# Optimization experiments

Hardware: AMD Instinct MI355X
Metric: run time of the kernel (lower is better)

The kernel has to match this reference:

```python
import jax, jax.numpy as jnp
import numpy as np

N_NODES = 50000
BN_EPS = 1e-5


def setup_inputs() -> dict:
    key = jax.random.key(0)
    ks = jax.random.split(key, 16)
    N, IN, H, OUT, E = N_NODES, 512, 128, 64, 800000
    s = lambda fi, fo: 1.0 / np.sqrt(fi)
    inp = {
        'x': jax.random.normal(ks[0], (N, IN), dtype=jnp.float32),
        'edge_index': jax.random.randint(ks[1], (2, E), 0, N, dtype=jnp.int32),
        # mlpA: Linear(N -> H)
        'WA': jax.random.uniform(ks[2], (H, N), jnp.float32, -s(N, H), s(N, H)),
        'bA': jax.random.uniform(ks[3], (H,), jnp.float32, -s(N, H), s(N, H)),
        # mlpX: Linear(IN -> H)
        'WX': jax.random.uniform(ks[4], (H, IN), jnp.float32, -s(IN, H), s(IN, H)),
        'bX': jax.random.uniform(ks[5], (H,), jnp.float32, -s(IN, H), s(IN, H)),
        # W: Linear(2H -> H)
        'W': jax.random.uniform(ks[6], (H, 2 * H), jnp.float32, -s(2 * H, H), s(2 * H, H)),
        'bW': jax.random.uniform(ks[7], (H,), jnp.float32, -s(2 * H, H), s(2 * H, H)),
        # mlp_final layer 1: Linear(H -> H) + BN
        'Wf1': jax.random.uniform(ks[8], (H, H), jnp.float32, -s(H, H), s(H, H)),
        'bf1': jax.random.uniform(ks[9], (H,), jnp.float32, -s(H, H), s(H, H)),
        'gamma': jnp.ones((H,), jnp.float32),
        'beta': jnp.zeros((H,), jnp.float32),
        # mlp_final layer 2: Linear(H -> OUT)
        'Wf2': jax.random.uniform(ks[10], (OUT, H), jnp.float32, -s(H, OUT), s(H, OUT)),
        'bf2': jax.random.uniform(ks[11], (OUT,), jnp.float32, -s(H, OUT), s(H, OUT)),
    }
    return inp


def _batchnorm(x, gamma, beta):
    # training-mode BN over the node/batch axis (biased variance, as in torch)
    mean = jnp.mean(x, axis=0)
    var = jnp.var(x, axis=0)
    return (x - mean) * jax.lax.rsqrt(var + BN_EPS) * gamma + beta


def reference(x, edge_index, WA, bA, WX, bX, W, bW, Wf1, bf1, gamma, beta, Wf2, bf2):
    row, col = edge_index[0], edge_index[1]
    row = row - row.min()
    # xA = A @ WA.T + bA  where A[i,j]=1 per (row,col) edge (duplicates sum).
    # Equivalent SpMM: gather columns of WA at `col`, segment-sum into `row`.
    xA = jax.ops.segment_sum(WA.T[col], row, num_segments=N_NODES) + bA  # [N, H]
    xX = x @ WX.T + bX  # [N, H]
    h = jnp.concatenate([xA, xX], axis=-1) @ W.T + bW  # [N, H]
    h = jax.nn.relu(h + xA + xX)
    # mlp_final (num_layers=2): Linear -> ReLU -> BN -> (dropout off) -> Linear
    h = jax.nn.relu(h @ Wf1.T + bf1)
    h = _batchnorm(h, gamma, beta)
    out = h @ Wf2.T + bf2  # [N, OUT]
    return out
```

## Files before the change

### kernel.cpp

```cpp
#include <hip/hip_runtime.h>

typedef __bf16 bf16_t;
typedef __bf16 bf16x8 __attribute__((ext_vector_type(8)));
typedef float f32x4 __attribute__((ext_vector_type(4)));

#define IN_DIM 512
#define H_DIM 128
#define OUT_DIM 64
#define BN_EPS 1e-5f
#define SCAN_BLK 2048

#define MFMA(a, b, c) __builtin_amdgcn_mfma_f32_16x16x32_bf16(a, b, c, 0, 0, 0)

__device__ __forceinline__ float ld_adapt(const void* p, size_t i, int isbf) {
    return isbf ? (float)((const bf16_t*)p)[i] : ((const float*)p)[i];
}

__device__ __forceinline__ void split8(const float* p, bf16x8& hi, bf16x8& lo) {
    f32x4 v0 = *(const f32x4*)p;
    f32x4 v1 = *(const f32x4*)(p + 4);
#pragma unroll
    for (int i = 0; i < 8; ++i) {
        float f = (i < 4) ? v0[i] : v1[i - 4];
        bf16_t h = (bf16_t)f;
        hi[i] = h;
        lo[i] = (bf16_t)(f - (float)h);
    }
}

__device__ __forceinline__ unsigned short bf16_bits(float f) {
    bf16_t h = (bf16_t)f;
    return __builtin_bit_cast(unsigned short, h);
}

__device__ __forceinline__ float2 bf2_unpack(unsigned v) {
    bf16_t lo = __builtin_bit_cast(bf16_t, (unsigned short)(v & 0xffffu));
    bf16_t hi = __builtin_bit_cast(bf16_t, (unsigned short)(v >> 16));
    return float2{(float)lo, (float)hi};
}

__global__ void k_init(const void* bA, const void* bX, const void* bW, const void* bf1,
                       const void* gamma, const void* beta, const void* bf2,
                       float* __restrict__ dst, int* __restrict__ flag) {
    __shared__ int s_isbf;
    if (threadIdx.x == 0) {
        unsigned u = *(const unsigned*)gamma;
        int f = (u == 0x3F803F80u) ? 1 : 0;
        *flag = f;
        s_isbf = f;
    }
    __syncthreads();
    int isbf = s_isbf;
    int t = threadIdx.x;
    dst[t] = ld_adapt(bA, t, isbf);
    dst[128 + t] = ld_adapt(bX, t, isbf);
    dst[256 + t] = ld_adapt(bW, t, isbf);
    dst[384 + t] = ld_adapt(bf1, t, isbf);
    dst[512 + t] = ld_adapt(gamma, t, isbf);
    dst[640 + t] = ld_adapt(beta, t, isbf);
    if (t < OUT_DIM) dst[768 + t] = ld_adapt(bf2, t, isbf);
}

__global__ __launch_bounds__(256) void k_transpose(const void* __restrict__ WA,
                                                   float* __restrict__ WAT, int N,
                                                   const int* __restrict__ flag) {
    __shared__ float t[64][130];
    int isbf = *flag;
    int n0 = blockIdx.x * 64;
    int tid = threadIdx.x;
#pragma unroll
    for (int i = 0; i < 32; ++i) {
        int lin = i * 256 + tid;
        int h = lin >> 6, nl = lin & 63;
        int n = n0 + nl;
        t[nl][h] = (n < N) ? ld_adapt(WA, (size_t)h * N + n, isbf) : 0.f;
    }
    __syncthreads();
    if (isbf) {
#pragma unroll
        for (int i = 0; i < 16; ++i) {
            int lin = i * 256 + tid;
            int nl = lin >> 6, hp = lin & 63;
            int n = n0 + nl;
            if (n < N) {
                unsigned u0 = bf16_bits(t[nl][hp * 2]);
                unsigned u1 = bf16_bits(t[nl][hp * 2 + 1]);
                ((unsigned*)WAT)[(size_t)n * 64 + hp] = u0 | (u1 << 16);
            }
        }
    } else {
#pragma unroll
        for (int i = 0; i < 32; ++i) {
            int lin = i * 256 + tid;
            int nl = lin >> 7, h = lin & 127;
            int n = n0 + nl;
            if (n < N) WAT[(size_t)n * H_DIM + h] = t[nl][h];
        }
    }
}

__global__ __launch_bounds__(256) void k_prep(const int* __restrict__ rows, int E,
                                              int* __restrict__ bmin, int* __restrict__ cnt,
                                              int* __restrict__ rank) {
    __shared__ int sm[4];
    int i = blockIdx.x * 256 + threadIdx.x;
    int m = 0x7fffffff;
    if (i < E) {
        int r = rows[i];
        m = r;
        rank[i] = atomicAdd(&cnt[r], 1);
    }
    for (int off = 32; off; off >>= 1) m = min(m, __shfl_xor(m, off, 64));
    if ((threadIdx.x & 63) == 0) sm[threadIdx.x >> 6] = m;
    __syncthreads();
    if (threadIdx.x == 0)
        bmin[blockIdx.x] = min(min(sm[0], sm[1]), min(sm[2], sm[3]));
}

__global__ __launch_bounds__(256) void k_scan1(const int* __restrict__ cnt,
                                               int* __restrict__ offs,
                                               int* __restrict__ bsum, int N) {
    __shared__ int ts[256];
    int base = blockIdx.x * SCAN_BLK;
    int t = threadIdx.x;
    int v[8], s = 0;
#pragma unroll
    for (int i = 0; i < 8; ++i) {
        int idx = base + t * 8 + i;
        v[i] = (idx < N) ? cnt[idx] : 0;
        s += v[i];
    }
    ts[t] = s;
    __syncthreads();
    for (int off = 1; off < 256; off <<= 1) {
        int x = (t >= off) ? ts[t - off] : 0;
        __syncthreads();
        ts[t] += x;
        __syncthreads();
    }
    int run = ts[t] - s;
#pragma unroll
    for (int i = 0; i < 8; ++i) {
        int idx = base + t * 8 + i;
        if (idx < N) offs[idx] = run;
        run += v[i];
    }
    if (t == 255) bsum[blockIdx.x] = ts[255];
}

__global__ __launch_bounds__(256) void k_scan2(int* __restrict__ bsum, int* __restrict__ offs,
                                               int NB, int N, const int* __restrict__ bmin,
                                               int nbmin, int* __restrict__ minbuf) {
    __shared__ int sm[256];
    int t = threadIdx.x;
    int m = 0x7fffffff;
    for (int i = t; i < nbmin; i += 256) m = min(m, bmin[i]);
    sm[t] = m;
    __syncthreads();
    for (int off = 128; off; off >>= 1) {
        if (t < off) sm[t] = min(sm[t], sm[t + off]);
        __syncthreads();
    }
    if (t == 0) {
        *minbuf = sm[0];
        int run = 0;
        for (int b = 0; b < NB; ++b) {
            int v = bsum[b];
            bsum[b] = run;
            run += v;
        }
        offs[N] = run;
    }
}

__global__ __launch_bounds__(256) void k_scan3(int* __restrict__ offs, const int* __restrict__ bsum,
                                               int N) {
    int i = blockIdx.x * 256 + threadIdx.x;
    if (i >= N) return;
    offs[i] += bsum[i / SCAN_BLK];
}

__global__ __launch_bounds__(256) void k_build(const int* __restrict__ rows,
                                               const int* __restrict__ cols, int E,
                                               const int* __restrict__ offs,
                                               const int* __restrict__ rank,
                                               int* __restrict__ scol) {
    int i = blockIdx.x * 256 + threadIdx.x;
    if (i >= E) return;
    int r = rows[i];
    int pos = offs[r] + rank[i];
    scol[pos] = cols[i];
}

__global__ __launch_bounds__(256) void k_gather(const int* __restrict__ offs,
                                                const int* __restrict__ scol,
                                                const float* __restrict__ WAT,
                                                const float* __restrict__ bA_f,
                                                const int* __restrict__ minbuf,
                                                const int* __restrict__ flag,
                                                float* __restrict__ xA, int N) {
    int wave = threadIdx.x >> 6, lane = threadIdx.x & 63;
    int r = blockIdx.x * 4 + wave;
    if (r >= N) return;
    int b = r + *minbuf;
    int isbf = *flag;
    int s = 0, e = 0;
    if (b < N) {
        s = offs[b];
        e = offs[b + 1];
    }
    float2 a0 = {0.f, 0.f}, a1 = {0.f, 0.f};
    int i = s;
    if (isbf) {
        const unsigned* Wb = (const unsigned*)WAT;
        for (; i + 3 < e; i += 4) {
            int c0 = scol[i], c1 = scol[i + 1], c2 = scol[i + 2], c3 = scol[i + 3];
            unsigned v0 = Wb[(size_t)c0 * 64 + lane];
            unsigned v1 = Wb[(size_t)c1 * 64 + lane];
            unsigned v2 = Wb[(size_t)c2 * 64 + lane];
            unsigned v3 = Wb[(size_t)c3 * 64 + lane];
            float2 w0 = bf2_unpack(v0), w1 = bf2_unpack(v1);
            float2 w2 = bf2_unpack(v2), w3 = bf2_unpack(v3);
            a0.x += w0.x + w2.x; a0.y += w0.y + w2.y;
            a1.x += w1.x + w3.x; a1.y += w1.y + w3.y;
        }
        for (; i < e; ++i) {
            float2 w = bf2_unpack(Wb[(size_t)scol[i] * 64 + lane]);
            a0.x += w.x; a0.y += w.y;
        }
    } else {
        for (; i + 3 < e; i += 4) {
            int c0 = scol[i], c1 = scol[i + 1], c2 = scol[i + 2], c3 = scol[i + 3];
            float2 w0 = *(const float2*)(WAT + (size_t)c0 * H_DIM + lane * 2);
            float2 w1 = *(const float2*)(WAT + (size_t)c1 * H_DIM + lane * 2);
            float2 w2 = *(const float2*)(WAT + (size_t)c2 * H_DIM + lane * 2);
            float2 w3 = *(const float2*)(WAT + (size_t)c3 * H_DIM + lane * 2);
            a0.x += w0.x + w2.x; a0.y += w0.y + w2.y;
            a1.x += w1.x + w3.x; a1.y += w1.y + w3.y;
        }
        for (; i < e; ++i) {
            int c = scol[i];
            float2 w = *(const float2*)(WAT + (size_t)c * H_DIM + lane * 2);
            a0.x += w.x; a0.y += w.y;
        }
    }
    float2 bias = *(const float2*)(bA_f + lane * 2);
    float2 out = {a0.x + a1.x + bias.x, a0.y + a1.y + bias.y};
    *(float2*)(xA + (size_t)r * H_DIM + lane * 2) = out;
}

__device__ __forceinline__ void pack_frag(const void* __restrict__ W, bf16_t* __restrict__ hi,
                                          bf16_t* __restrict__ lo, int K, int NC,
                                          int addres, int isbf, int f, int lane) {
    int ks = f / (NC >> 4), nt = f % (NC >> 4);
    int n = nt * 16 + (lane & 15);
    int k0 = ks * 32 + (lane >> 4) * 8;
    bf16_t* dh = hi + (size_t)f * 512 + lane * 8;
    bf16_t* dl = lo + (size_t)f * 512 + lane * 8;
#pragma unroll
    for (int j = 0; j < 8; ++j) {
        int kk = k0 + j;
        float v = ld_adapt(W, (size_t)n * K + kk, isbf);
        if (addres && (kk == n || kk == n + H_DIM)) v += 1.f;
        bf16_t h = (bf16_t)v;
        dh[j] = h;
        dl[j] = (bf16_t)(v - (float)h);
    }
}

__global__ __launch_bounds__(256) void k_pack3(const void* WX, bf16_t* WXh, bf16_t* WXl,
                                               const void* W, bf16_t* Wh, bf16_t* Wl,
                                               const void* Wf1, bf16_t* Wf1h, bf16_t* Wf1l,
                                               const int* __restrict__ flag) {
    int g = blockIdx.x * 256 + threadIdx.x;
    int f = g >> 6, lane = g & 63;
    int isbf = *flag;
    if (f < 128)
        pack_frag(WX, WXh, WXl, IN_DIM, H_DIM, 0, isbf, f, lane);
    else if (f < 192)
        pack_frag(W, Wh, Wl, 2 * H_DIM, H_DIM, isbf ? 0 : 1, isbf, f - 128, lane);
    else if (f < 224)
        pack_frag(Wf1, Wf1h, Wf1l, H_DIM, H_DIM, 0, isbf, f - 192, lane);
}

template <int ISBF>
__device__ __forceinline__ void fuseA_body(
    const void* __restrict__ x, const float* __restrict__ xAf,
    const bf16_t* __restrict__ WXh, const bf16_t* __restrict__ WXl,
    const bf16_t* __restrict__ Wh, const bf16_t* __restrict__ Wl,
    const bf16_t* __restrict__ Wf1h, const bf16_t* __restrict__ Wf1l,
    const float* __restrict__ smallf, float* __restrict__ h2, int M,
    float* __restrict__ ax, float* __restrict__ ls_sum, float* __restrict__ ls_sq) {
    int tid = threadIdx.x;
    int wave = tid >> 6, lane = tid & 63, l16 = lane & 15, quad = lane >> 4;
    int mbase = blockIdx.x * 64 + wave * 16;
    int r0 = min(mbase + l16, M - 1);
    const float* bX = smallf + 128;
    const float* bW = smallf + 256;
    const float* bf1 = smallf + 384;

    f32x4 acc[8];
#pragma unroll
    for (int nt = 0; nt < 8; ++nt) acc[nt] = f32x4{0.f, 0.f, 0.f, 0.f};
    if (ISBF) {
        size_t offx = (size_t)r0 * IN_DIM + quad * 8;
        for (int ks = 0; ks < 16; ++ks) {
            bf16x8 ah = *(const bf16x8*)((const bf16_t*)x + offx + ks * 32);
            const bf16_t* bhp = WXh + (size_t)ks * 8 * 512 + lane * 8;
#pragma unroll
            for (int nt = 0; nt < 8; ++nt) {
                bf16x8 bh = *(const bf16x8*)(bhp + nt * 512);
                acc[nt] = MFMA(ah, bh, acc[nt]);
            }
        }
    } else {
        size_t offx = (size_t)r0 * IN_DIM + quad * 8;
        for (int ks = 0; ks < 16; ++ks) {
            bf16x8 ah, al;
            split8((const float*)x + offx + ks * 32, ah, al);
            const bf16_t* bhp = WXh + (size_t)ks * 8 * 512 + lane * 8;
            const bf16_t* blp = WXl + (size_t)ks * 8 * 512 + lane * 8;
#pragma unroll
            for (int nt = 0; nt < 8; ++nt) {
                bf16x8 bh = *(const bf16x8*)(bhp + nt * 512);
                bf16x8 bl = *(const bf16x8*)(blp + nt * 512);
                acc[nt] = MFMA(ah, bh, acc[nt]);
                acc[nt] = MFMA(ah, bl, acc[nt]);
                acc[nt] = MFMA(al, bh, acc[nt]);
            }
        }
    }
#pragma unroll
    for (int nt = 0; nt < 8; ++nt) {
        int col = nt * 16 + l16;
        float b = bX[col];
#pragma unroll
        for (int r = 0; r < 4; ++r) {
            int lr = quad * 4 + r;
            ax[lr * 132 + col] = acc[nt][r] + b;
        }
    }

#pragma unroll
    for (int nt = 0; nt < 8; ++nt) acc[nt] = f32x4{0.f, 0.f, 0.f, 0.f};
    for (int ks = 0; ks < 8; ++ks) {
        bf16x8 ah, al;
        if (ks < 4)
            split8(xAf + (size_t)r0 * H_DIM + ks * 32 + quad * 8, ah, al);
        else
            split8(ax + l16 * 132 + (ks - 4) * 32 + quad * 8, ah, al);
        const bf16_t* bhp = Wh + (size_t)ks * 8 * 512 + lane * 8;
        if (ISBF) {
#pragma unroll
            for (int nt = 0; nt < 8; ++nt) {
                bf16x8 bh = *(const bf16x8*)(bhp + nt * 512);
                acc[nt] = MFMA(ah, bh, acc[nt]);
                acc[nt] = MFMA(al, bh, acc[nt]);
            }
        } else {
            const bf16_t* blp = Wl + (size_t)ks * 8 * 512 + lane * 8;
#pragma unroll
            for (int nt = 0; nt < 8; ++nt) {
                bf16x8 bh = *(const bf16x8*)(bhp + nt * 512);
                bf16x8 bl = *(const bf16x8*)(blp + nt * 512);
                acc[nt] = MFMA(ah, bh, acc[nt]);
                acc[nt] = MFMA(ah, bl, acc[nt]);
                acc[nt] = MFMA(al, bh, acc[nt]);
            }
        }
    }
    if (ISBF) {
#pragma unroll
        for (int nt = 0; nt < 8; ++nt) {
            int col = nt * 16 + l16;
            float b = bW[col];
#pragma unroll
            for (int r = 0; r < 4; ++r) {
                int lr = quad * 4 + r;
                int rr = min(mbase + lr, M - 1);
                float resid = xAf[(size_t)rr * H_DIM + col] + ax[lr * 132 + col];
                ax[lr * 132 + col] = fmaxf(acc[nt][r] + b + resid, 0.f);
            }
        }
    } else {
#pragma unroll
        for (int nt = 0; nt < 8; ++nt) {
            int col = nt * 16 + l16;
            float b = bW[col];
#pragma unroll
            for (int r = 0; r < 4; ++r) {
                int lr = quad * 4 + r;
                ax[lr * 132 + col] = fmaxf(acc[nt][r] + b, 0.f);
            }
        }
    }

#pragma unroll
    for (int nt = 0; nt < 8; ++nt) acc[nt] = f32x4{0.f, 0.f, 0.f, 0.f};
    for (int ks = 0; ks < 4; ++ks) {
        bf16x8 ah, al;
        split8(ax + l16 * 132 + ks * 32 + quad * 8, ah, al);
        const bf16_t* bhp = Wf1h + (size_t)ks * 8 * 512 + lane * 8;
        if (ISBF) {
#pragma unroll
            for (int nt = 0; nt < 8; ++nt) {
                bf16x8 bh = *(const bf16x8*)(bhp + nt * 512);
                acc[nt] = MFMA(ah, bh, acc[nt]);
                acc[nt] = MFMA(al, bh, acc[nt]);
            }
        } else {
            const bf16_t* blp = Wf1l + (size_t)ks * 8 * 512 + lane * 8;
#pragma unroll
            for (int nt = 0; nt < 8; ++nt) {
                bf16x8 bh = *(const bf16x8*)(bhp + nt * 512);
                bf16x8 bl = *(const bf16x8*)(blp + nt * 512);
                acc[nt] = MFMA(ah, bh, acc[nt]);
                acc[nt] = MFMA(ah, bl, acc[nt]);
                acc[nt] = MFMA(al, bh, acc[nt]);
            }
        }
    }
#pragma unroll
    for (int nt = 0; nt < 8; ++nt) {
        int col = nt * 16 + l16;
        float b = bf1[col];
        float s = 0.f, s2 = 0.f;
#pragma unroll
        for (int r = 0; r < 4; ++r) {
            int row = mbase + quad * 4 + r;
            if (row < M) {
                float v = fmaxf(acc[nt][r] + b, 0.f);
                h2[(size_t)row * H_DIM + col] = v;
                s += v;
                s2 += v * v;
            }
        }
        s += __shfl_xor(s, 16, 64);
        s += __shfl_xor(s, 32, 64);
        s2 += __shfl_xor(s2, 16, 64);
        s2 += __shfl_xor(s2, 32, 64);
        if (quad == 0) {
            atomicAdd(&ls_sum[col], s);
            atomicAdd(&ls_sq[col], s2);
        }
    }
}

__global__ __launch_bounds__(256) void k_fuseA(
    const void* __restrict__ x, const float* __restrict__ xAf,
    const bf16_t* __restrict__ WXh, const bf16_t* __restrict__ WXl,
    const bf16_t* __restrict__ Wh, const bf16_t* __restrict__ Wl,
    const bf16_t* __restrict__ Wf1h, const bf16_t* __restrict__ Wf1l,
    const float* __restrict__ smallf, float* __restrict__ h2,
    double* __restrict__ sums, double* __restrict__ sumsq,
    const int* __restrict__ flag, int M) {
    __shared__ float axx[4][16 * 132];
    __shared__ float ls_sum[H_DIM], ls_sq[H_DIM];
    int tid = threadIdx.x;
    if (tid < H_DIM) {
        ls_sum[tid] = 0.f;
        ls_sq[tid] = 0.f;
    }
    __syncthreads();
    float* ax = axx[tid >> 6];
    if (*flag)
        fuseA_body<1>(x, xAf, WXh, WXl, Wh, Wl, Wf1h, Wf1l, smallf, h2, M, ax, ls_sum, ls_sq);
    else
        fuseA_body<0>(x, xAf, WXh, WXl, Wh, Wl, Wf1h, Wf1l, smallf, h2, M, ax, ls_sum, ls_sq);
    __syncthreads();
    if (tid < H_DIM) {
        atomicAdd(&sums[tid], (double)ls_sum[tid]);
        atomicAdd(&sumsq[tid], (double)ls_sq[tid]);
    }
}

__global__ __launch_bounds__(256) void k_packB(
    const void* __restrict__ Wf2, const float* __restrict__ smallf,
    const double* __restrict__ sums, const double* __restrict__ sumsq,
    bf16_t* __restrict__ W2h, bf16_t* __restrict__ W2l,
    float* __restrict__ b2g, const int* __restrict__ flag, int M) {
    __shared__ float aw[H_DIM], cw[H_DIM];
    int t = threadIdx.x;
    int isbf = *flag;
    const float* gamma_f = smallf + 512;
    const float* beta_f = smallf + 640;
    const float* bf2_f = smallf + 768;
    if (t < H_DIM) {
        double mean = sums[t] / (double)M;
        double var = sumsq[t] / (double)M - mean * mean;
        if (var < 0) var = 0;
        float a = gamma_f[t] * rsqrtf((float)var + BN_EPS);
        aw[t] = a;
        cw[t] = beta_f[t] - (float)mean * a;
    }
    __syncthreads();
    if (t < OUT_DIM) {
        float acc = bf2_f[t];
        for (int j = 0; j < H_DIM; ++j) acc += ld_adapt(Wf2, (size_t)t * H_DIM + j, isbf) * cw[j];
        b2g[t] = acc;
    }
    for (int u = t; u < 1024; u += 256) {
        int f = u >> 6, ln = u & 63;
        int ks = f >> 2, nt = f & 3;
        int n = nt * 16 + (ln & 15);
        int k0 = ks * 32 + (ln >> 4) * 8;
#pragma unroll
        for (int j = 0; j < 8; ++j) {
            float v = ld_adapt(Wf2, (size_t)n * H_DIM + k0 + j, isbf) * aw[k0 + j];
            bf16_t h = (bf16_t)v;
            W2h[f * 512 + ln * 8 + j] = h;
            W2l[f * 512 + ln * 8 + j] = (bf16_t)(v - (float)h);
        }
    }
}

__global__ __launch_bounds__(256) void k_fuseB(
    const float* __restrict__ h2, const bf16_t* __restrict__ W2h,
    const bf16_t* __restrict__ W2l, const float* __restrict__ b2g,
    void* __restrict__ outv, const int* __restrict__ flag, int M) {
    int t = threadIdx.x;
    int isbf = *flag;
    int wave = t >> 6, lane = t & 63, l16 = lane & 15, quad = lane >> 4;
    int mbase = blockIdx.x * 64 + wave * 16;
    int r0 = min(mbase + l16, M - 1);
    f32x4 acc4[4];
#pragma unroll
    for (int nt = 0; nt < 4; ++nt) acc4[nt] = f32x4{0.f, 0.f, 0.f, 0.f};
    for (int ks = 0; ks < 4; ++ks) {
        bf16x8 ah, al;
        split8(h2 + (size_t)r0 * H_DIM + ks * 32 + quad * 8, ah, al);
#pragma unroll
        for (int nt = 0; nt < 4; ++nt) {
            bf16x8 bh = *(const bf16x8*)(W2h + (ks * 4 + nt) * 512 + lane * 8);
            bf16x8 bl = *(const bf16x8*)(W2l + (ks * 4 + nt) * 512 + lane * 8);
            acc4[nt] = MFMA(ah, bh, acc4[nt]);
            acc4[nt] = MFMA(ah, bl, acc4[nt]);
            acc4[nt] = MFMA(al, bh, acc4[nt]);
        }
    }
#pragma unroll
    for (int nt = 0; nt < 4; ++nt) {
        int col = nt * 16 + l16;
        float b = b2g[col];
#pragma unroll
        for (int r = 0; r < 4; ++r) {
            int row = mbase + quad * 4 + r;
            if (row < M) {
                float v = acc4[nt][r] + b;
                if (isbf)
                    ((bf16_t*)outv)[(size_t)row * OUT_DIM + col] = (bf16_t)v;
                else
                    ((float*)outv)[(size_t)row * OUT_DIM + col] = v;
            }
        }
    }
}

extern "C" void kernel_launch(void* const* d_in, const int* in_sizes, int n_in,
                              void* d_out, int out_size, void* d_ws, size_t ws_size,
                              hipStream_t stream) {
    const void* x = d_in[0];
    const int* ei = (const int*)d_in[1];
    const void* WA = d_in[2];
    const void* bA = d_in[3];
    const void* WX = d_in[4];
    const void* bX = d_in[5];
    const void* W = d_in[6];
    const void* bW = d_in[7];
    const void* Wf1 = d_in[8];
    const void* bf1 = d_in[9];
    const void* gamma = d_in[10];
    const void* beta = d_in[11];
    const void* Wf2 = d_in[12];
    const void* bf2 = d_in[13];

    const int N = in_sizes[0] / IN_DIM;
    const int E = in_sizes[1] / 2;
    const int* rows = ei;
    const int* cols = ei + E;
    const int eblocks = (E + 255) / 256;

    char* ws = (char*)d_ws;
    size_t off = 0;
    auto alloc = [&](size_t bytes) {
        char* p = ws + off;
        off += (bytes + 255) & ~(size_t)255;
        return p;
    };
    int* flag = (int*)alloc(4);
    int* minbuf = (int*)alloc(4);
    float* smallf = (float*)alloc(832 * 4);
    double* sums = (double*)alloc(2 * H_DIM * 8);
    double* sumsq = sums + H_DIM;
    bf16_t* WXp_h = (bf16_t*)alloc((size_t)IN_DIM * H_DIM * 2);
    bf16_t* WXp_l = (bf16_t*)alloc((size_t)IN_DIM * H_DIM * 2);
    bf16_t* Wp_h = (bf16_t*)alloc((size_t)256 * H_DIM * 2);
    bf16_t* Wp_l = (bf16_t*)alloc((size_t)256 * H_DIM * 2);
    bf16_t* Wf1p_h = (bf16_t*)alloc((size_t)H_DIM * H_DIM * 2);
    bf16_t* Wf1p_l = (bf16_t*)alloc((size_t)H_DIM * H_DIM * 2);
    bf16_t* W2h = (bf16_t*)alloc((size_t)16 * 512 * 2);
    bf16_t* W2l = (bf16_t*)alloc((size_t)16 * 512 * 2);
    float* b2g = (float*)alloc(OUT_DIM * 4);
    int* cnt = (int*)alloc((size_t)N * 4);
    int* offs = (int*)alloc(((size_t)N + 1) * 4);
    int* rank = (int*)alloc((size_t)E * 4);
    int* bsum = (int*)alloc(64 * 4);
    int* bmin = (int*)alloc((size_t)eblocks * 4);
    int* scol = (int*)alloc((size_t)E * 4);
    float* WAT = (float*)alloc((size_t)N * H_DIM * 4);
    float* xAf = (float*)alloc((size_t)N * H_DIM * 4);
    float* h2 = WAT;

    float* bA_f = smallf + 0;

    hipMemsetAsync(cnt, 0, (size_t)N * 4, stream);
    hipMemsetAsync(sums, 0, 2 * H_DIM * 8, stream);

    k_init<<<1, 128, 0, stream>>>(bA, bX, bW, bf1, gamma, beta, bf2, smallf, flag);
    k_transpose<<<(N + 63) / 64, 256, 0, stream>>>(WA, WAT, N, flag);
    k_pack3<<<56, 256, 0, stream>>>(WX, WXp_h, WXp_l, W, Wp_h, Wp_l, Wf1, Wf1p_h, Wf1p_l, flag);

    k_prep<<<eblocks, 256, 0, stream>>>(rows, E, bmin, cnt, rank);
    int NB = (N + SCAN_BLK - 1) / SCAN_BLK;
    k_scan1<<<NB, 256, 0, stream>>>(cnt, offs, bsum, N);
    k_scan2<<<1, 256, 0, stream>>>(bsum, offs, NB, N, bmin, eblocks, minbuf);
    k_scan3<<<(N + 255) / 256, 256, 0, stream>>>(offs, bsum, N);
    k_build<<<eblocks, 256, 0, stream>>>(rows, cols, E, offs, rank, scol);
    k_gather<<<(N + 3) / 4, 256, 0, stream>>>(offs, scol, WAT, bA_f, minbuf, flag, xAf, N);

    int fblocks = (N + 63) / 64;
    k_fuseA<<<fblocks, 256, 0, stream>>>(x, xAf, WXp_h, WXp_l, Wp_h, Wp_l, Wf1p_h, Wf1p_l,
                                         smallf, h2, sums, sumsq, flag, N);
    k_packB<<<1, 256, 0, stream>>>(Wf2, smallf, sums, sumsq, W2h, W2l, b2g, flag, N);
    k_fuseB<<<fblocks, 256, 0, stream>>>(h2, W2h, W2l, b2g, d_out, flag, N);
}
```

Measured before the change: 457.2 us.

## Split fused MLP block across waves by output columns with banked BN atomics

Each k_fuseA block now handles 16 rows instead of 64, and its four waves split the 128 output columns (two 16-column tiles each) instead of each wave owning its own 16 rows. The shared activation tile is shared across the block with __syncthreads between stages, and launch bounds request higher occupancy. Per-block shared-memory BN reduction is replaced by direct double atomics into 8 banks indexed by block, and k_packB sums the banks. This lowers registers per thread and raises block count and occupancy, but every wave now reloads the same x rows, and the change adds barriers and four times as many global atomics.

Result: slower. 472.1 us (+3.3%).

```diff
diff --git a/kernel.cpp b/kernel.cpp
--- a/kernel.cpp
+++ b/kernel.cpp
@@ -289,147 +289,128 @@
     const bf16_t* __restrict__ WXh, const bf16_t* __restrict__ WXl,
     const bf16_t* __restrict__ Wh, const bf16_t* __restrict__ Wl,
     const bf16_t* __restrict__ Wf1h, const bf16_t* __restrict__ Wf1l,
-    const float* __restrict__ smallf, float* __restrict__ h2, int M,
-    float* __restrict__ ax, float* __restrict__ ls_sum, float* __restrict__ ls_sq) {
+    const float* __restrict__ smallf, float* __restrict__ h2,
+    double* __restrict__ sums, double* __restrict__ sumsq, int M,
+    float* __restrict__ ax) {
     int tid = threadIdx.x;
     int wave = tid >> 6, lane = tid & 63, l16 = lane & 15, quad = lane >> 4;
-    int mbase = blockIdx.x * 64 + wave * 16;
+    int mbase = blockIdx.x * 16;
     int r0 = min(mbase + l16, M - 1);
+    int nt0 = wave * 2;
     const float* bX = smallf + 128;
     const float* bW = smallf + 256;
     const float* bf1 = smallf + 384;
 
-    f32x4 acc[8];
-#pragma unroll
-    for (int nt = 0; nt < 8; ++nt) acc[nt] = f32x4{0.f, 0.f, 0.f, 0.f};
-    if (ISBF) {
-        size_t offx = (size_t)r0 * IN_DIM + quad * 8;
-        for (int ks = 0; ks < 16; ++ks) {
-            bf16x8 ah = *(const bf16x8*)((const bf16_t*)x + offx + ks * 32);
-            const bf16_t* bhp = WXh + (size_t)ks * 8 * 512 + lane * 8;
-#pragma unroll
-            for (int nt = 0; nt < 8; ++nt) {
-                bf16x8 bh = *(const bf16x8*)(bhp + nt * 512);
-                acc[nt] = MFMA(ah, bh, acc[nt]);
-            }
-        }
-    } else {
+    f32x4 acc[2];
+    acc[0] = f32x4{0.f, 0.f, 0.f, 0.f};
+    acc[1] = f32x4{0.f, 0.f, 0.f, 0.f};
+
+    {
         size_t offx = (size_t)r0 * IN_DIM + quad * 8;
         for (int ks = 0; ks < 16; ++ks) {
             bf16x8 ah, al;
-            split8((const float*)x + offx + ks * 32, ah, al);
-            const bf16_t* bhp = WXh + (size_t)ks * 8 * 512 + lane * 8;
-            const bf16_t* blp = WXl + (size_t)ks * 8 * 512 + lane * 8;
-#pragma unroll
-            for (int nt = 0; nt < 8; ++nt) {
-                bf16x8 bh = *(const bf16x8*)(bhp + nt * 512);
-                bf16x8 bl = *(const bf16x8*)(blp + nt * 512);
-                acc[nt] = MFMA(ah, bh, acc[nt]);
-                acc[nt] = MFMA(ah, bl, acc[nt]);
-                acc[nt] = MFMA(al, bh, acc[nt]);
-            }
-        }
-    }
-#pragma unroll
-    for (int nt = 0; nt < 8; ++nt) {
-        int col = nt * 16 + l16;
+            if (ISBF) {
+                ah = *(const bf16x8*)((const bf16_t*)x + offx + ks * 32);
+            } else {
+                split8((const float*)x + offx + ks * 32, ah, al);
+            }
+#pragma unroll
+            for (int ntl = 0; ntl < 2; ++ntl) {
+                size_t fo = (size_t)(ks * 8 + nt0 + ntl) * 512 + lane * 8;
+                bf16x8 bh = *(const bf16x8*)(WXh + fo);
+                acc[ntl] = MFMA(ah, bh, acc[ntl]);
+                if (!ISBF) {
+                    bf16x8 bl = *(const bf16x8*)(WXl + fo);
+                    acc[ntl] = MFMA(ah, bl, acc[ntl]);
+                    acc[ntl] = MFMA(al, bh, acc[ntl]);
+                }
+            }
+        }
+    }
+#pragma unroll
+    for (int ntl = 0; ntl < 2; ++ntl) {
+        int col = (nt0 + ntl) * 16 + l16;
         float b = bX[col];
 #pragma unroll
         for (int r = 0; r < 4; ++r) {
             int lr = quad * 4 + r;
-            ax[lr * 132 + col] = acc[nt][r] + b;
-        }
-    }
-
-#pragma unroll
-    for (int nt = 0; nt < 8; ++nt) acc[nt] = f32x4{0.f, 0.f, 0.f, 0.f};
+            ax[lr * 132 + col] = acc[ntl][r] + b;
+        }
+    }
+    __syncthreads();
+
+    acc[0] = f32x4{0.f, 0.f, 0.f, 0.f};
+    acc[1] = f32x4{0.f, 0.f, 0.f, 0.f};
     for (int ks = 0; ks < 8; ++ks) {
         bf16x8 ah, al;
         if (ks < 4)
             split8(xAf + (size_t)r0 * H_DIM + ks * 32 + quad * 8, ah, al);
         else
             split8(ax + l16 * 132 + (ks - 4) * 32 + quad * 8, ah, al);
-        const bf16_t* bhp = Wh + (size_t)ks * 8 * 512 + lane * 8;
-        if (ISBF) {
-#pragma unroll
-            for (int nt = 0; nt < 8; ++nt) {
-                bf16x8 bh = *(const bf16x8*)(bhp + nt * 512);
-                acc[nt] = MFMA(ah, bh, acc[nt]);
-                acc[nt] = MFMA(al, bh, acc[nt]);
-            }
-        } else {
-            const bf16_t* blp = Wl + (size_t)ks * 8 * 512 + lane * 8;
-#pragma unroll
-            for (int nt = 0; nt < 8; ++nt) {
-                bf16x8 bh = *(const bf16x8*)(bhp + nt * 512);
-                bf16x8 bl = *(const bf16x8*)(blp + nt * 512);
-                acc[nt] = MFMA(ah, bh, acc[nt]);
-                acc[nt] = MFMA(ah, bl, acc[nt]);
-                acc[nt] = MFMA(al, bh, acc[nt]);
-            }
-        }
-    }
-    if (ISBF) {
-#pragma unroll
-        for (int nt = 0; nt < 8; ++nt) {
-            int col = nt * 16 + l16;
-            float b = bW[col];
-#pragma unroll
-            for (int r = 0; r < 4; ++r) {
-                int lr = quad * 4 + r;
+#pragma unroll
+        for (int ntl = 0; ntl < 2; ++ntl) {
+            size_t fo = (size_t)(ks * 8 + nt0 + ntl) * 512 + lane * 8;
+            bf16x8 bh = *(const bf16x8*)(Wh + fo);
+            if (ISBF) {
+                acc[ntl] = MFMA(ah, bh, acc[ntl]);
+                acc[ntl] = MFMA(al, bh, acc[ntl]);
+            } else {
+                bf16x8 bl = *(const bf16x8*)(Wl + fo);
+                acc[ntl] = MFMA(ah, bh, acc[ntl]);
+                acc[ntl] = MFMA(ah, bl, acc[ntl]);
+                acc[ntl] = MFMA(al, bh, acc[ntl]);
+            }
+        }
+    }
+    __syncthreads();
+#pragma unroll
+    for (int ntl = 0; ntl < 2; ++ntl) {
+        int col = (nt0 + ntl) * 16 + l16;
+        float b = bW[col];
+#pragma unroll
+        for (int r = 0; r < 4; ++r) {
+            int lr = quad * 4 + r;
+            float v = acc[ntl][r] + b;
+            if (ISBF) {
                 int rr = min(mbase + lr, M - 1);
-                float resid = xAf[(size_t)rr * H_DIM + col] + ax[lr * 132 + col];
-                ax[lr * 132 + col] = fmaxf(acc[nt][r] + b + resid, 0.f);
-            }
-        }
-    } else {
-#pragma unroll
-        for (int nt = 0; nt < 8; ++nt) {
-            int col = nt * 16 + l16;
-            float b = bW[col];
-#pragma unroll
-            for (int r = 0; r < 4; ++r) {
-                int lr = quad * 4 + r;
-                ax[lr * 132 + col] = fmaxf(acc[nt][r] + b, 0.f);
-            }
-        }
-    }
-
-#pragma unroll
-    for (int nt = 0; nt < 8; ++nt) acc[nt] = f32x4{0.f, 0.f, 0.f, 0.f};
+                v += xAf[(size_t)rr * H_DIM + col] + ax[lr * 132 + col];
+            }
+            ax[lr * 132 + col] = fmaxf(v, 0.f);
+        }
+    }
+    __syncthreads();
+
+    acc[0] = f32x4{0.f, 0.f, 0.f, 0.f};
+    acc[1] = f32x4{0.f, 0.f, 0.f, 0.f};
     for (int ks = 0; ks < 4; ++ks) {
         bf16x8 ah, al;
         split8(ax + l16 * 132 + ks * 32 + quad * 8, ah, al);
-        const bf16_t* bhp = Wf1h + (size_t)ks * 8 * 512 + lane * 8;
-        if (ISBF) {
-#pragma unroll
-            for (int nt = 0; nt < 8; ++nt) {
-                bf16x8 bh = *(const bf16x8*)(bhp + nt * 512);
-                acc[nt] = MFMA(ah, bh, acc[nt]);
-                acc[nt] = MFMA(al, bh, acc[nt]);
-            }
-        } else {
-            const bf16_t* blp = Wf1l + (size_t)ks * 8 * 512 + lane * 8;
-#pragma unroll
-            for (int nt = 0; nt < 8; ++nt) {
-                bf16x8 bh = *(const bf16x8*)(bhp + nt * 512);
-                bf16x8 bl = *(const bf16x8*)(blp + nt * 512);
-                acc[nt] = MFMA(ah, bh, acc[nt]);
-                acc[nt] = MFMA(ah, bl, acc[nt]);
-                acc[nt] = MFMA(al, bh, acc[nt]);
-            }
-        }
-    }
-#pragma unroll
-    for (int nt = 0; nt < 8; ++nt) {
-        int col = nt * 16 + l16;
+#pragma unroll
+        for (int ntl = 0; ntl < 2; ++ntl) {
+            size_t fo = (size_t)(ks * 8 + nt0 + ntl) * 512 + lane * 8;
+            bf16x8 bh = *(const bf16x8*)(Wf1h + fo);
+            if (ISBF) {
+                acc[ntl] = MFMA(ah, bh, acc[ntl]);
+                acc[ntl] = MFMA(al, bh, acc[ntl]);
+            } else {
+                bf16x8 bl = *(const bf16x8*)(Wf1l + fo);
+                acc[ntl] = MFMA(ah, bh, acc[ntl]);
+                acc[ntl] = MFMA(ah, bl, acc[ntl]);
+                acc[ntl] = MFMA(al, bh, acc[ntl]);
+            }
+        }
+    }
+    int bank = (blockIdx.x & 7) * H_DIM;
+#pragma unroll
+    for (int ntl = 0; ntl < 2; ++ntl) {
+        int col = (nt0 + ntl) * 16 + l16;
         float b = bf1[col];
         float s = 0.f, s2 = 0.f;
 #pragma unroll
         for (int r = 0; r < 4; ++r) {
             int row = mbase + quad * 4 + r;
             if (row < M) {
-                float v = fmaxf(acc[nt][r] + b, 0.f);
+                float v = fmaxf(acc[ntl][r] + b, 0.f);
                 h2[(size_t)row * H_DIM + col] = v;
                 s += v;
                 s2 += v * v;
@@ -440,13 +421,13 @@
         s2 += __shfl_xor(s2, 16, 64);
         s2 += __shfl_xor(s2, 32, 64);
         if (quad == 0) {
-            atomicAdd(&ls_sum[col], s);
-            atomicAdd(&ls_sq[col], s2);
-        }
-    }
-}
-
-__global__ __launch_bounds__(256) void k_fuseA(
+            atomicAdd(&sums[bank + col], (double)s);
+            atomicAdd(&sumsq[bank + col], (double)s2);
+        }
+    }
+}
+
+__global__ __launch_bounds__(256, 8) void k_fuseA(
     const void* __restrict__ x, const float* __restrict__ xAf,
     const bf16_t* __restrict__ WXh, const bf16_t* __restrict__ WXl,
     const bf16_t* __restrict__ Wh, const bf16_t* __restrict__ Wl,
@@ -454,24 +435,11 @@
     const float* __restrict__ smallf, float* __restrict__ h2,
     double* __restrict__ sums, double* __restrict__ sumsq,
     const int* __restrict__ flag, int M) {
-    __shared__ float axx[4][16 * 132];
-    __shared__ float ls_sum[H_DIM], ls_sq[H_DIM];
-    int tid = threadIdx.x;
-    if (tid < H_DIM) {
-        ls_sum[tid] = 0.f;
-        ls_sq[tid] = 0.f;
-    }
-    __syncthreads();
-    float* ax = axx[tid >> 6];
+    __shared__ float ax[16 * 132];
     if (*flag)
-        fuseA_body<1>(x, xAf, WXh, WXl, Wh, Wl, Wf1h, Wf1l, smallf, h2, M, ax, ls_sum, ls_sq);
+        fuseA_body<1>(x, xAf, WXh, WXl, Wh, Wl, Wf1h, Wf1l, smallf, h2, sums, sumsq, M, ax);
     else
-        fuseA_body<0>(x, xAf, WXh, WXl, Wh, Wl, Wf1h, Wf1l, smallf, h2, M, ax, ls_sum, ls_sq);
-    __syncthreads();
-    if (tid < H_DIM) {
-        atomicAdd(&sums[tid], (double)ls_sum[tid]);
-        atomicAdd(&sumsq[tid], (double)ls_sq[tid]);
-    }
+        fuseA_body<0>(x, xAf, WXh, WXl, Wh, Wl, Wf1h, Wf1l, smallf, h2, sums, sumsq, M, ax);
 }
 
 __global__ __launch_bounds__(256) void k_packB(
@@ -486,8 +454,14 @@
     const float* beta_f = smallf + 640;
     const float* bf2_f = smallf + 768;
     if (t < H_DIM) {
-        double mean = sums[t] / (double)M;
-        double var = sumsq[t] / (double)M - mean * mean;
+        double ssum = 0.0, ssq = 0.0;
+#pragma unroll
+        for (int bk = 0; bk < 8; ++bk) {
+            ssum += sums[bk * H_DIM + t];
+            ssq += sumsq[bk * H_DIM + t];
+        }
+        double mean = ssum / (double)M;
+        double var = ssq / (double)M - mean * mean;
         if (var < 0) var = 0;
         float a = gamma_f[t] * rsqrtf((float)var + BN_EPS);
         aw[t] = a;
@@ -590,8 +564,8 @@
     int* flag = (int*)alloc(4);
     int* minbuf = (int*)alloc(4);
     float* smallf = (float*)alloc(832 * 4);
-    double* sums = (double*)alloc(2 * H_DIM * 8);
-    double* sumsq = sums + H_DIM;
+    double* sums = (double*)alloc(2 * 8 * H_DIM * 8);
+    double* sumsq = sums + 8 * H_DIM;
     bf16_t* WXp_h = (bf16_t*)alloc((size_t)IN_DIM * H_DIM * 2);
     bf16_t* WXp_l = (bf16_t*)alloc((size_t)IN_DIM * H_DIM * 2);
     bf16_t* Wp_h = (bf16_t*)alloc((size_t)256 * H_DIM * 2);
@@ -614,7 +588,7 @@
     float* bA_f = smallf + 0;
 
     hipMemsetAsync(cnt, 0, (size_t)N * 4, stream);
-    hipMemsetAsync(sums, 0, 2 * H_DIM * 8, stream);
+    hipMemsetAsync(sums, 0, 2 * 8 * H_DIM * 8, stream);
 
     k_init<<<1, 128, 0, stream>>>(bA, bX, bW, bf1, gamma, beta, bf2, smallf, flag);
     k_transpose<<<(N + 63) / 64, 256, 0, stream>>>(WA, WAT, N, flag);
@@ -628,9 +602,10 @@
     k_build<<<eblocks, 256, 0, stream>>>(rows, cols, E, offs, rank, scol);
     k_gather<<<(N + 3) / 4, 256, 0, stream>>>(offs, scol, WAT, bA_f, minbuf, flag, xAf, N);
 
-    int fblocks = (N + 63) / 64;
-    k_fuseA<<<fblocks, 256, 0, stream>>>(x, xAf, WXp_h, WXp_l, Wp_h, Wp_l, Wf1p_h, Wf1p_l,
-                                         smallf, h2, sums, sumsq, flag, N);
+    int fblocksA = (N + 15) / 16;
+    k_fuseA<<<fblocksA, 256, 0, stream>>>(x, xAf, WXp_h, WXp_l, Wp_h, Wp_l, Wf1p_h, Wf1p_l,
+                                          smallf, h2, sums, sumsq, flag, N);
     k_packB<<<1, 256, 0, stream>>>(Wf2, smallf, sums, sumsq, W2h, W2l, b2g, flag, N);
-    k_fuseB<<<fblocks, 256, 0, stream>>>(h2, W2h, W2l, b2g, d_out, flag, N);
-}
+    int fblocksB = (N + 63) / 64;
+    k_fuseB<<<fblocksB, 256, 0, stream>>>(h2, W2h, W2l, b2g, d_out, flag, N);
+}
```

## Process two 16-row tiles per wave in fused MLP kernel to reuse weight fragments

Applied to the files above, without the earlier changes.

Each wave in k_fuseA now computes 32 rows instead of 16, holding two sets of accumulators so every loaded weight fragment (hi/lo) feeds two MFMAs. Blocks shrink to 128 threads (2 waves) while still covering 64 rows, halving total weight fragment loads from global/L2. The cost is doubled accumulator register pressure (64 extra VGPRs), which may reduce occupancy, and fewer waves per block.

Result: faster. 435.1 us (-4.8%).

```diff
diff --git a/kernel.cpp b/kernel.cpp
--- a/kernel.cpp
+++ b/kernel.cpp
@@ -293,40 +293,46 @@
     float* __restrict__ ax, float* __restrict__ ls_sum, float* __restrict__ ls_sq) {
     int tid = threadIdx.x;
     int wave = tid >> 6, lane = tid & 63, l16 = lane & 15, quad = lane >> 4;
-    int mbase = blockIdx.x * 64 + wave * 16;
+    int mbase = blockIdx.x * 64 + wave * 32;
     int r0 = min(mbase + l16, M - 1);
+    int r1 = min(mbase + 16 + l16, M - 1);
     const float* bX = smallf + 128;
     const float* bW = smallf + 256;
     const float* bf1 = smallf + 384;
 
-    f32x4 acc[8];
-#pragma unroll
-    for (int nt = 0; nt < 8; ++nt) acc[nt] = f32x4{0.f, 0.f, 0.f, 0.f};
-    if (ISBF) {
-        size_t offx = (size_t)r0 * IN_DIM + quad * 8;
+    f32x4 acc0[8], acc1[8];
+#pragma unroll
+    for (int nt = 0; nt < 8; ++nt) {
+        acc0[nt] = f32x4{0.f, 0.f, 0.f, 0.f};
+        acc1[nt] = f32x4{0.f, 0.f, 0.f, 0.f};
+    }
+
+    {
+        size_t offx0 = (size_t)r0 * IN_DIM + quad * 8;
+        size_t offx1 = (size_t)r1 * IN_DIM + quad * 8;
         for (int ks = 0; ks < 16; ++ks) {
-            bf16x8 ah = *(const bf16x8*)((const bf16_t*)x + offx + ks * 32);
+            bf16x8 ah0, al0, ah1, al1;
+            if (ISBF) {
+                ah0 = *(const bf16x8*)((const bf16_t*)x + offx0 + ks * 32);
+                ah1 = *(const bf16x8*)((const bf16_t*)x + offx1 + ks * 32);
+            } else {
+                split8((const float*)x + offx0 + ks * 32, ah0, al0);
+                split8((const float*)x + offx1 + ks * 32, ah1, al1);
+            }
             const bf16_t* bhp = WXh + (size_t)ks * 8 * 512 + lane * 8;
+            const bf16_t* blp = WXl + (size_t)ks * 8 * 512 + lane * 8;
 #pragma unroll
             for (int nt = 0; nt < 8; ++nt) {
                 bf16x8 bh = *(const bf16x8*)(bhp + nt * 512);
-                acc[nt] = MFMA(ah, bh, acc[nt]);
-            }
-        }
-    } else {
-        size_t offx = (size_t)r0 * IN_DIM + quad * 8;
-        for (int ks = 0; ks < 16; ++ks) {
-            bf16x8 ah, al;
-            split8((const float*)x + offx + ks * 32, ah, al);
-            const bf16_t* bhp = WXh + (size_t)ks * 8 * 512 + lane * 8;
-            const bf16_t* blp = WXl + (size_t)ks * 8 * 512 + lane * 8;
-#pragma unroll
-            for (int nt = 0; nt < 8; ++nt) {
-                bf16x8 bh = *(const bf16x8*)(bhp + nt * 512);
-                bf16x8 bl = *(const bf16x8*)(blp + nt * 512);
-                acc[nt] = MFMA(ah, bh, acc[nt]);
-                acc[nt] = MFMA(ah, bl, acc[nt]);
-                acc[nt] = MFMA(al, bh, acc[nt]);
+                acc0[nt] = MFMA(ah0, bh, acc0[nt]);
+                acc1[nt] = MFMA(ah1, bh, acc1[nt]);
+                if (!ISBF) {
+                    bf16x8 bl = *(const bf16x8*)(blp + nt * 512);
+                    acc0[nt] = MFMA(ah0, bl, acc0[nt]);
+                    acc0[nt] = MFMA(al0, bh, acc0[nt]);
+                    acc1[nt] = MFMA(ah1, bl, acc1[nt]);
+                    acc1[nt] = MFMA(al1, bh, acc1[nt]);
+                }
             }
         }
     }
@@ -337,86 +343,83 @@
 #pragma unroll
         for (int r = 0; r < 4; ++r) {
             int lr = quad * 4 + r;
-            ax[lr * 132 + col] = acc[nt][r] + b;
-        }
-    }
-
-#pragma unroll
-    for (int nt = 0; nt < 8; ++nt) acc[nt] = f32x4{0.f, 0.f, 0.f, 0.f};
+            ax[lr * 132 + col] = acc0[nt][r] + b;
+            ax[(16 + lr) * 132 + col] = acc1[nt][r] + b;
+        }
+    }
+
+#pragma unroll
+    for (int nt = 0; nt < 8; ++nt) {
+        acc0[nt] = f32x4{0.f, 0.f, 0.f, 0.f};
+        acc1[nt] = f32x4{0.f, 0.f, 0.f, 0.f};
+    }
     for (int ks = 0; ks < 8; ++ks) {
-        bf16x8 ah, al;
-        if (ks < 4)
-            split8(xAf + (size_t)r0 * H_DIM + ks * 32 + quad * 8, ah, al);
-        else
-            split8(ax + l16 * 132 + (ks - 4) * 32 + quad * 8, ah, al);
+        bf16x8 ah0, al0, ah1, al1;
+        if (ks < 4) {
+            split8(xAf + (size_t)r0 * H_DIM + ks * 32 + quad * 8, ah0, al0);
+            split8(xAf + (size_t)r1 * H_DIM + ks * 32 + quad * 8, ah1, al1);
+        } else {
+            split8(ax + l16 * 132 + (ks - 4) * 32 + quad * 8, ah0, al0);
+            split8(ax + (16 + l16) * 132 + (ks - 4) * 32 + quad * 8, ah1, al1);
+        }
         const bf16_t* bhp = Wh + (size_t)ks * 8 * 512 + lane * 8;
-        if (ISBF) {
-#pragma unroll
-            for (int nt = 0; nt < 8; ++nt) {
-                bf16x8 bh = *(const bf16x8*)(bhp + nt * 512);
-                acc[nt] = MFMA(ah, bh, acc[nt]);
-                acc[nt] = MFMA(al, bh, acc[nt]);
-            }
-        } else {
-            const bf16_t* blp = Wl + (size_t)ks * 8 * 512 + lane * 8;
-#pragma unroll
-            for (int nt = 0; nt < 8; ++nt) {
-                bf16x8 bh = *(const bf16x8*)(bhp + nt * 512);
+        const bf16_t* blp = Wl + (size_t)ks * 8 * 512 + lane * 8;
+#pragma unroll
+        for (int nt = 0; nt < 8; ++nt) {
+            bf16x8 bh = *(const bf16x8*)(bhp + nt * 512);
+            acc0[nt] = MFMA(ah0, bh, acc0[nt]);
+            acc1[nt] = MFMA(ah1, bh, acc1[nt]);
+            acc0[nt] = MFMA(al0, bh, acc0[nt]);
+            acc1[nt] = MFMA(al1, bh, acc1[nt]);
+            if (!ISBF) {
                 bf16x8 bl = *(const bf16x8*)(blp + nt * 512);
-                acc[nt] = MFMA(ah, bh, acc[nt]);
-                acc[nt] = MFMA(ah, bl, acc[nt]);
-                acc[nt] = MFMA(al, bh, acc[nt]);
-            }
-        }
-    }
-    if (ISBF) {
+                acc0[nt] = MFMA(ah0, bl, acc0[nt]);
+                acc1[nt] = MFMA(ah1, bl, acc1[nt]);
+            }
+        }
+    }
+#pragma unroll
+    for (int nt = 0; nt < 8; ++nt) {
+        int col = nt * 16 + l16;
+        float b = bW[col];
+#pragma unroll
+        for (int r = 0; r < 4; ++r) {
+            int lr = quad * 4 + r;
+            float v0 = acc0[nt][r] + b;
+            float v1 = acc1[nt][r] + b;
+            if (ISBF) {
+                int rr0 = min(mbase + lr, M - 1);
+                int rr1 = min(mbase + 16 + lr, M - 1);
+                v0 += xAf[(size_t)rr0 * H_DIM + col] + ax[lr * 132 + col];
+                v1 += xAf[(size_t)rr1 * H_DIM + col] + ax[(16 + lr) * 132 + col];
+            }
+            ax[lr * 132 + col] = fmaxf(v0, 0.f);
+            ax[(16 + lr) * 132 + col] = fmaxf(v1, 0.f);
+        }
+    }
+
+#pragma unroll
+    for (int nt = 0; nt < 8; ++nt) {
+        acc0[nt] = f32x4{0.f, 0.f, 0.f, 0.f};
+        acc1[nt] = f32x4{0.f, 0.f, 0.f, 0.f};
+    }
+    for (int ks = 0; ks < 4; ++ks) {
+        bf16x8 ah0, al0, ah1, al1;
+        split8(ax + l16 * 132 + ks * 32 + quad * 8, ah0, al0);
+        split8(ax + (16 + l16) * 132 + ks * 32 + quad * 8, ah1, al1);
+        const bf16_t* bhp = Wf1h + (size_t)ks * 8 * 512 + lane * 8;
+        const bf16_t* blp = Wf1l + (size_t)ks * 8 * 512 + lane * 8;
 #pragma unroll
         for (int nt = 0; nt < 8; ++nt) {
-            int col = nt * 16 + l16;
-            float b = bW[col];
-#pragma unroll
-            for (int r = 0; r < 4; ++r) {
-                int lr = quad * 4 + r;
-                int rr = min(mbase + lr, M - 1);
-                float resid = xAf[(size_t)rr * H_DIM + col] + ax[lr * 132 + col];
-                ax[lr * 132 + col] = fmaxf(acc[nt][r] + b + resid, 0.f);
-            }
-        }
-    } else {
-#pragma unroll
-        for (int nt = 0; nt < 8; ++nt) {
-            int col = nt * 16 + l16;
-            float b = bW[col];
-#pragma unroll
-            for (int r = 0; r < 4; ++r) {
-                int lr = quad * 4 + r;
-                ax[lr * 132 + col] = fmaxf(acc[nt][r] + b, 0.f);
-            }
-        }
-    }
-
-#pragma unroll
-    for (int nt = 0; nt < 8; ++nt) acc[nt] = f32x4{0.f, 0.f, 0.f, 0.f};
-    for (int ks = 0; ks < 4; ++ks) {
-        bf16x8 ah, al;
-        split8(ax + l16 * 132 + ks * 32 + quad * 8, ah, al);
-        const bf16_t* bhp = Wf1h + (size_t)ks * 8 * 512 + lane * 8;
-        if (ISBF) {
-#pragma unroll
-            for (int nt = 0; nt < 8; ++nt) {
-                bf16x8 bh = *(const bf16x8*)(bhp + nt * 512);
-                acc[nt] = MFMA(ah, bh, acc[nt]);
-                acc[nt] = MFMA(al, bh, acc[nt]);
-            }
-        } else {
-            const bf16_t* blp = Wf1l + (size_t)ks * 8 * 512 + lane * 8;
-#pragma unroll
-            for (int nt = 0; nt < 8; ++nt) {
-                bf16x8 bh = *(const bf16x8*)(bhp + nt * 512);
+            bf16x8 bh = *(const bf16x8*)(bhp + nt * 512);
+            acc0[nt] = MFMA(ah0, bh, acc0[nt]);
+            acc1[nt] = MFMA(ah1, bh, acc1[nt]);
+            acc0[nt] = MFMA(al0, bh, acc0[nt]);
+            acc1[nt] = MFMA(al1, bh, acc1[nt]);
+            if (!ISBF) {
                 bf16x8 bl = *(const bf16x8*)(blp + nt * 512);
-                acc[nt] = MFMA(ah, bh, acc[nt]);
-                acc[nt] = MFMA(ah, bl, acc[nt]);
-                acc[nt] = MFMA(al, bh, acc[nt]);
+                acc0[nt] = MFMA(ah0, bl, acc0[nt]);
+                acc1[nt] = MFMA(ah1, bl, acc1[nt]);
             }
         }
     }
@@ -427,10 +430,17 @@
         float s = 0.f, s2 = 0.f;
 #pragma unroll
         for (int r = 0; r < 4; ++r) {
-            int row = mbase + quad * 4 + r;
-            if (row < M) {
-                float v = fmaxf(acc[nt][r] + b, 0.f);
-                h2[(size_t)row * H_DIM + col] = v;
+            int row0 = mbase + quad * 4 + r;
+            if (row0 < M) {
+                float v = fmaxf(acc0[nt][r] + b, 0.f);
+                h2[(size_t)row0 * H_DIM + col] = v;
+                s += v;
+                s2 += v * v;
+            }
+            int row1 = mbase + 16 + quad * 4 + r;
+            if (row1 < M) {
+                float v = fmaxf(acc1[nt][r] + b, 0.f);
+                h2[(size_t)row1 * H_DIM + col] = v;
                 s += v;
                 s2 += v * v;
             }
@@ -446,7 +456,7 @@
     }
 }
 
-__global__ __launch_bounds__(256) void k_fuseA(
+__global__ __launch_bounds__(128) void k_fuseA(
     const void* __restrict__ x, const float* __restrict__ xAf,
     const bf16_t* __restrict__ WXh, const bf16_t* __restrict__ WXl,
     const bf16_t* __restrict__ Wh, const bf16_t* __restrict__ Wl,
@@ -454,13 +464,11 @@
     const float* __restrict__ smallf, float* __restrict__ h2,
     double* __restrict__ sums, double* __restrict__ sumsq,
     const int* __restrict__ flag, int M) {
-    __shared__ float axx[4][16 * 132];
+    __shared__ float axx[2][32 * 132];
     __shared__ float ls_sum[H_DIM], ls_sq[H_DIM];
     int tid = threadIdx.x;
-    if (tid < H_DIM) {
-        ls_sum[tid] = 0.f;
-        ls_sq[tid] = 0.f;
-    }
+    ls_sum[tid] = 0.f;
+    ls_sq[tid] = 0.f;
     __syncthreads();
     float* ax = axx[tid >> 6];
     if (*flag)
@@ -468,10 +476,8 @@
     else
         fuseA_body<0>(x, xAf, WXh, WXl, Wh, Wl, Wf1h, Wf1l, smallf, h2, M, ax, ls_sum, ls_sq);
     __syncthreads();
-    if (tid < H_DIM) {
-        atomicAdd(&sums[tid], (double)ls_sum[tid]);
-        atomicAdd(&sumsq[tid], (double)ls_sq[tid]);
-    }
+    atomicAdd(&sums[tid], (double)ls_sum[tid]);
+    atomicAdd(&sumsq[tid], (double)ls_sq[tid]);
 }
 
 __global__ __launch_bounds__(256) void k_packB(
@@ -628,9 +634,10 @@
     k_build<<<eblocks, 256, 0, stream>>>(rows, cols, E, offs, rank, scol);
     k_gather<<<(N + 3) / 4, 256, 0, stream>>>(offs, scol, WAT, bA_f, minbuf, flag, xAf, N);
 
-    int fblocks = (N + 63) / 64;
-    k_fuseA<<<fblocks, 256, 0, stream>>>(x, xAf, WXp_h, WXp_l, Wp_h, Wp_l, Wf1p_h, Wf1p_l,
-                                         smallf, h2, sums, sumsq, flag, N);
+    int fblocksA = (N + 63) / 64;
+    k_fuseA<<<fblocksA, 128, 0, stream>>>(x, xAf, WXp_h, WXp_l, Wp_h, Wp_l, Wf1p_h, Wf1p_l,
+                                          smallf, h2, sums, sumsq, flag, N);
     k_packB<<<1, 256, 0, stream>>>(Wf2, smallf, sums, sumsq, W2h, W2l, b2g, flag, N);
-    k_fuseB<<<fblocks, 256, 0, stream>>>(h2, W2h, W2l, b2g, d_out, flag, N);
-}
+    int fblocksB = (N + 63) / 64;
+    k_fuseB<<<fblocksB, 256, 0, stream>>>(h2, W2h, W2l, b2g, d_out, flag, N);
+}
```
